# Kernel tuning notes

Hardware: AMD Instinct MI355X
Metric: run time of the kernel (lower is better)

Reference implementation:

```python
import jax, jax.numpy as jnp
import numpy as np

_THR = 0.008856  # OpenCV Lab threshold (6/29)^3


def _f_lab(t):
    # f(t) = t^(1/3) if t > thr else 7.787*t + 16/116 ; safe-where avoids nan/inf grads at 0
    safe = jnp.where(t > _THR, t, 1.0)
    return jnp.where(t > _THR, jnp.cbrt(safe), 7.787 * t + 16.0 / 116.0)


def _rgb_to_lab(img):
    """img: [B,3,H,W] in [0,1] -> OpenCV 8-bit-scaled Lab, divided by 255 (as in the torch code)."""
    img = jnp.clip(img, 0.0, 1.0)  # blur mixes channels so values can exceed 1; cv2 path saturates to 8-bit range
    r, g, b = img[:, 0], img[:, 1], img[:, 2]
    # linear RGB -> XYZ (OpenCV matrix), with white-point normalization of X and Z
    X = (0.412453 * r + 0.357580 * g + 0.180423 * b) / 0.950456
    Y = 0.212671 * r + 0.715160 * g + 0.072169 * b
    Z = (0.019334 * r + 0.119193 * g + 0.950227 * b) / 1.088754
    fX, fY, fZ = _f_lab(X), _f_lab(Y), _f_lab(Z)
    safeY = jnp.where(Y > _THR, Y, 1.0)
    L = jnp.where(Y > _THR, 116.0 * jnp.cbrt(safeY) - 16.0, 903.3 * Y)
    a = 500.0 * (fX - fY) + 128.0
    bb = 200.0 * (fY - fZ) + 128.0
    # OpenCV 8-bit scaling: L*255/100, a+128, b+128 ; torch code then divides by 255
    lab = jnp.stack([L * 255.0 / 100.0, a, bb], axis=1) / 255.0
    return lab


def _blur(img, weight):
    # F.conv2d with ones(3,3,5,5)/25, padding=2: each output channel is the SUM over input
    # channels of the 5x5 mean (full channel mixing, as in the torch module).
    return jax.lax.conv_general_dilated(
        img, weight, window_strides=(1, 1), padding=[(2, 2), (2, 2)],
        dimension_numbers=("NCHW", "OIHW", "NCHW"))


def setup_inputs() -> dict:
    key = jax.random.key(0)
    k1, k2 = jax.random.split(key)
    B, C, H, W = 32, 3, 512, 512
    img1 = jax.random.uniform(k1, (B, C, H, W), dtype=jnp.float32)
    img2 = jax.random.uniform(k2, (B, C, H, W), dtype=jnp.float32)
    kernel_size = 5
    weight = jnp.ones((3, 3, kernel_size, kernel_size), dtype=jnp.float32) / (kernel_size ** 2)
    return {"img1": img1, "img2": img2, "weight": weight}


def reference(img1, img2, weight):
    lab1 = _rgb_to_lab(_blur(img1, weight))
    lab2 = _rgb_to_lab(_blur(img2, weight))
    return jnp.mean((lab1 - lab2) ** 2)  # F.mse_loss, reduction='mean'
```

## Files before the change

### kernel.cpp

```cpp
#include <hip/hip_runtime.h>


constexpr int TILE  = 64;
constexpr int HALO  = 2;
constexpr int ROWS  = TILE + 2 * HALO;
constexpr int CPAD  = 72;
constexpr int NF4   = CPAD / 4;
constexpr int IMG_H = 512;
constexpr int IMG_W = 512;
constexpr int BATCH = 32;
constexpr float THR = 0.008856f;

__global__ __launch_bounds__(256, 8)
void lcol_mse_kernel(const float* __restrict__ img1,
                     const float* __restrict__ img2,
                     const float* __restrict__ weight,
                     float* __restrict__ out)
{
    __shared__ float cs[ROWS * CPAD];
    __shared__ float wpart[4];

    const int tid = threadIdx.x;
    const int bx0 = blockIdx.x * TILE;
    const int by0 = blockIdx.y * TILE;
    const int b   = blockIdx.z;
    const float wtap = weight[0];

    const size_t plane = (size_t)IMG_H * IMG_W;
    const float* bases[2] = { img1 + (size_t)b * 3 * plane,
                              img2 + (size_t)b * 3 * plane };

    const int x  = tid & 63;
    const int r0 = (tid >> 6) * 16;

    float L1[16];
    float acc = 0.f;

    for (int img = 0; img < 2; ++img) {
        const float* base = bases[img];

        for (int n = tid; n < ROWS * NF4; n += 256) {
            int row = n / NF4;
            int k   = n - row * NF4;
            int gy  = by0 + row - HALO;
            int gx  = bx0 + 4 * k - 4;
            float4 v = make_float4(0.f, 0.f, 0.f, 0.f);
            if ((unsigned)gy < (unsigned)IMG_H && (unsigned)gx < (unsigned)IMG_W) {
                const float* p = base + (size_t)gy * IMG_W + gx;
                float4 r  = *(const float4*)(p);
                float4 g  = *(const float4*)(p + plane);
                float4 bl = *(const float4*)(p + 2 * plane);
                v = make_float4(r.x + g.x + bl.x, r.y + g.y + bl.y,
                                r.z + g.z + bl.z, r.w + g.w + bl.w);
            }
            *(float4*)&cs[row * CPAD + 4 * k] = v;
        }
        __syncthreads();

        const float* colbase = &cs[x + 2];
        float h0 = colbase[(r0    ) * CPAD] + colbase[(r0    ) * CPAD + 1] + colbase[(r0    ) * CPAD + 2] + colbase[(r0    ) * CPAD + 3] + colbase[(r0    ) * CPAD + 4];
        float h1 = colbase[(r0 + 1) * CPAD] + colbase[(r0 + 1) * CPAD + 1] + colbase[(r0 + 1) * CPAD + 2] + colbase[(r0 + 1) * CPAD + 3] + colbase[(r0 + 1) * CPAD + 4];
        float h2 = colbase[(r0 + 2) * CPAD] + colbase[(r0 + 2) * CPAD + 1] + colbase[(r0 + 2) * CPAD + 2] + colbase[(r0 + 2) * CPAD + 3] + colbase[(r0 + 2) * CPAD + 4];
        float h3 = colbase[(r0 + 3) * CPAD] + colbase[(r0 + 3) * CPAD + 1] + colbase[(r0 + 3) * CPAD + 2] + colbase[(r0 + 3) * CPAD + 3] + colbase[(r0 + 3) * CPAD + 4];
        #pragma unroll
        for (int k = 0; k < 16; ++k) {
            const float* p = colbase + (r0 + 4 + k) * CPAD;
            float h4 = p[0] + p[1] + p[2] + p[3] + p[4];
            float v  = (h0 + h1 + h2 + h3 + h4) * wtap;
            v = fminf(fmaxf(v, 0.f), 1.f);
            float L = (v > THR) ? (116.f * cbrtf(v) - 16.f) : (903.3f * v);
            if (img == 0) L1[k] = L;
            else { float d = L1[k] - L; acc += d * d; }
            h0 = h1; h1 = h2; h2 = h3; h3 = h4;
        }
        __syncthreads();
    }

    #pragma unroll
    for (int off = 32; off; off >>= 1) acc += __shfl_down(acc, off);
    if ((tid & 63) == 0) wpart[tid >> 6] = acc;
    __syncthreads();
    if (tid == 0) {
        float s = wpart[0] + wpart[1] + wpart[2] + wpart[3];
        const float scale = (float)(1.0 / (10000.0 * (double)BATCH * 3.0 * IMG_H * IMG_W));
        atomicAdd(out, s * scale);
    }
}

extern "C" void kernel_launch(void* const* d_in, const int* in_sizes, int n_in,
                              void* d_out, int out_size, void* d_ws, size_t ws_size,
                              hipStream_t stream) {
    const float* img1   = (const float*)d_in[0];
    const float* img2   = (const float*)d_in[1];
    const float* weight = (const float*)d_in[2];
    float* out = (float*)d_out;

    hipMemsetAsync(out, 0, sizeof(float), stream);

    dim3 grid(IMG_W / TILE, IMG_H / TILE, BATCH);
    lcol_mse_kernel<<<grid, dim3(256), 0, stream>>>(img1, img2, weight, out);
}
```

Baseline: 235.0 us.

## Double-buffer LDS tiles and process two tiles per block with prefetch

Halves the grid so each block handles two tiles, which means four image-tile units per block. The shared-memory tile is double-buffered: global loads for the next unit are issued into registers before computing the current one, then written to the other buffer. This aims to hide global memory latency behind the cbrt/blur compute. In exchange it raises register pressure, lowers the occupancy target from 8 to 4 blocks per CU, and uses fewer blocks overall.

```diff
diff --git a/kernel.cpp b/kernel.cpp
--- a/kernel.cpp
+++ b/kernel.cpp
@@ -6,73 +6,122 @@
 constexpr int ROWS  = TILE + 2 * HALO;
 constexpr int CPAD  = 72;
 constexpr int NF4   = CPAD / 4;
+constexpr int NITER = ROWS * NF4;
 constexpr int IMG_H = 512;
 constexpr int IMG_W = 512;
 constexpr int BATCH = 32;
+constexpr int NBLOCKS = 1024;
 constexpr float THR = 0.008856f;
 
-__global__ __launch_bounds__(256, 8)
+__device__ __forceinline__ void issue_loads(const float* __restrict__ base,
+                                            int by0, int bx0, int tid,
+                                            float4 rv[5], float4 gv[5], float4 bv[5])
+{
+    const size_t plane = (size_t)IMG_H * IMG_W;
+    #pragma unroll
+    for (int k = 0; k < 5; ++k) {
+        int n    = tid + 256 * k;
+        int row  = n / NF4;
+        int col4 = (n - row * NF4) * 4;
+        int gy   = by0 + row - HALO;
+        int gx   = bx0 + col4 - 4;
+        float4 z = make_float4(0.f, 0.f, 0.f, 0.f);
+        rv[k] = z; gv[k] = z; bv[k] = z;
+        if (n < NITER && (unsigned)gy < (unsigned)IMG_H && (unsigned)gx < (unsigned)IMG_W) {
+            const float* p = base + (size_t)gy * IMG_W + gx;
+            rv[k] = *(const float4*)(p);
+            gv[k] = *(const float4*)(p + plane);
+            bv[k] = *(const float4*)(p + 2 * plane);
+        }
+    }
+}
+
+__device__ __forceinline__ void write_stage(float* __restrict__ buf, int tid,
+                                            const float4 rv[5], const float4 gv[5],
+                                            const float4 bv[5])
+{
+    #pragma unroll
+    for (int k = 0; k < 5; ++k) {
+        int n = tid + 256 * k;
+        if (n < NITER) {
+            int row  = n / NF4;
+            int col4 = (n - row * NF4) * 4;
+            float4 v;
+            v.x = rv[k].x + gv[k].x + bv[k].x;
+            v.y = rv[k].y + gv[k].y + bv[k].y;
+            v.z = rv[k].z + gv[k].z + bv[k].z;
+            v.w = rv[k].w + gv[k].w + bv[k].w;
+            *(float4*)&buf[row * CPAD + col4] = v;
+        }
+    }
+}
+
+__device__ __forceinline__ void compute_unit(const float* __restrict__ buf,
+                                             int x, int r0, float wtap, bool first,
+                                             float L1[16], float& acc)
+{
+    const float* colbase = buf + x + 2;
+    float h0 = colbase[(r0    ) * CPAD] + colbase[(r0    ) * CPAD + 1] + colbase[(r0    ) * CPAD + 2] + colbase[(r0    ) * CPAD + 3] + colbase[(r0    ) * CPAD + 4];
+    float h1 = colbase[(r0 + 1) * CPAD] + colbase[(r0 + 1) * CPAD + 1] + colbase[(r0 + 1) * CPAD + 2] + colbase[(r0 + 1) * CPAD + 3] + colbase[(r0 + 1) * CPAD + 4];
+    float h2 = colbase[(r0 + 2) * CPAD] + colbase[(r0 + 2) * CPAD + 1] + colbase[(r0 + 2) * CPAD + 2] + colbase[(r0 + 2) * CPAD + 3] + colbase[(r0 + 2) * CPAD + 4];
+    float h3 = colbase[(r0 + 3) * CPAD] + colbase[(r0 + 3) * CPAD + 1] + colbase[(r0 + 3) * CPAD + 2] + colbase[(r0 + 3) * CPAD + 3] + colbase[(r0 + 3) * CPAD + 4];
+    #pragma unroll
+    for (int k = 0; k < 16; ++k) {
+        const float* p = colbase + (r0 + 4 + k) * CPAD;
+        float h4 = p[0] + p[1] + p[2] + p[3] + p[4];
+        float v  = (h0 + h1 + h2 + h3 + h4) * wtap;
+        v = fminf(fmaxf(v, 0.f), 1.f);
+        float L = (v > THR) ? (116.f * cbrtf(v) - 16.f) : (903.3f * v);
+        if (first) L1[k] = L;
+        else { float d = L1[k] - L; acc += d * d; }
+        h0 = h1; h1 = h2; h2 = h3; h3 = h4;
+    }
+}
+
+__global__ __launch_bounds__(256, 4)
 void lcol_mse_kernel(const float* __restrict__ img1,
                      const float* __restrict__ img2,
                      const float* __restrict__ weight,
                      float* __restrict__ out)
 {
-    __shared__ float cs[ROWS * CPAD];
+    __shared__ float cs[2][ROWS * CPAD];
     __shared__ float wpart[4];
 
     const int tid = threadIdx.x;
-    const int bx0 = blockIdx.x * TILE;
-    const int by0 = blockIdx.y * TILE;
-    const int b   = blockIdx.z;
+    const int x   = tid & 63;
+    const int r0  = (tid >> 6) * 16;
     const float wtap = weight[0];
+    const size_t plane = (size_t)IMG_H * IMG_W;
 
-    const size_t plane = (size_t)IMG_H * IMG_W;
-    const float* bases[2] = { img1 + (size_t)b * 3 * plane,
-                              img2 + (size_t)b * 3 * plane };
-
-    const int x  = tid & 63;
-    const int r0 = (tid >> 6) * 16;
+    int by0s[2], bx0s[2];
+    const float* bases[4];
+    #pragma unroll
+    for (int t = 0; t < 2; ++t) {
+        int tile = (int)blockIdx.x + t * NBLOCKS;
+        int b    = tile >> 6;
+        int rem  = tile & 63;
+        by0s[t]  = (rem >> 3) * TILE;
+        bx0s[t]  = (rem & 7) * TILE;
+        bases[2 * t]     = img1 + (size_t)b * 3 * plane;
+        bases[2 * t + 1] = img2 + (size_t)b * 3 * plane;
+    }
 
     float L1[16];
     float acc = 0.f;
+    float4 rv[5], gv[5], bv[5];
 
-    for (int img = 0; img < 2; ++img) {
-        const float* base = bases[img];
+    issue_loads(bases[0], by0s[0], bx0s[0], tid, rv, gv, bv);
+    write_stage(cs[0], tid, rv, gv, bv);
+    __syncthreads();
 
-        for (int n = tid; n < ROWS * NF4; n += 256) {
-            int row = n / NF4;
-            int k   = n - row * NF4;
-            int gy  = by0 + row - HALO;
-            int gx  = bx0 + 4 * k - 4;
-            float4 v = make_float4(0.f, 0.f, 0.f, 0.f);
-            if ((unsigned)gy < (unsigned)IMG_H && (unsigned)gx < (unsigned)IMG_W) {
-                const float* p = base + (size_t)gy * IMG_W + gx;
-                float4 r  = *(const float4*)(p);
-                float4 g  = *(const float4*)(p + plane);
-                float4 bl = *(const float4*)(p + 2 * plane);
-                v = make_float4(r.x + g.x + bl.x, r.y + g.y + bl.y,
-                                r.z + g.z + bl.z, r.w + g.w + bl.w);
-            }
-            *(float4*)&cs[row * CPAD + 4 * k] = v;
-        }
-        __syncthreads();
-
-        const float* colbase = &cs[x + 2];
-        float h0 = colbase[(r0    ) * CPAD] + colbase[(r0    ) * CPAD + 1] + colbase[(r0    ) * CPAD + 2] + colbase[(r0    ) * CPAD + 3] + colbase[(r0    ) * CPAD + 4];
-        float h1 = colbase[(r0 + 1) * CPAD] + colbase[(r0 + 1) * CPAD + 1] + colbase[(r0 + 1) * CPAD + 2] + colbase[(r0 + 1) * CPAD + 3] + colbase[(r0 + 1) * CPAD + 4];
-        float h2 = colbase[(r0 + 2) * CPAD] + colbase[(r0 + 2) * CPAD + 1] + colbase[(r0 + 2) * CPAD + 2] + colbase[(r0 + 2) * CPAD + 3] + colbase[(r0 + 2) * CPAD + 4];
-        float h3 = colbase[(r0 + 3) * CPAD] + colbase[(r0 + 3) * CPAD + 1] + colbase[(r0 + 3) * CPAD + 2] + colbase[(r0 + 3) * CPAD + 3] + colbase[(r0 + 3) * CPAD + 4];
-        #pragma unroll
-        for (int k = 0; k < 16; ++k) {
-            const float* p = colbase + (r0 + 4 + k) * CPAD;
-            float h4 = p[0] + p[1] + p[2] + p[3] + p[4];
-            float v  = (h0 + h1 + h2 + h3 + h4) * wtap;
-            v = fminf(fmaxf(v, 0.f), 1.f);
-            float L = (v > THR) ? (116.f * cbrtf(v) - 16.f) : (903.3f * v);
-            if (img == 0) L1[k] = L;
-            else { float d = L1[k] - L; acc += d * d; }
-            h0 = h1; h1 = h2; h2 = h3; h3 = h4;
-        }
+    #pragma unroll
+    for (int u = 0; u < 4; ++u) {
+        if (u < 3)
+            issue_loads(bases[u + 1], by0s[(u + 1) >> 1], bx0s[(u + 1) >> 1],
+                        tid, rv, gv, bv);
+        compute_unit(cs[u & 1], x, r0, wtap, (u & 1) == 0, L1, acc);
+        if (u < 3)
+            write_stage(cs[(u + 1) & 1], tid, rv, gv, bv);
         __syncthreads();
     }
 
@@ -97,6 +146,5 @@
 
     hipMemsetAsync(out, 0, sizeof(float), stream);
 
-    dim3 grid(IMG_W / TILE, IMG_H / TILE, BATCH);
-    lcol_mse_kernel<<<grid, dim3(256), 0, stream>>>(img1, img2, weight, out);
+    lcol_mse_kernel<<<dim3(NBLOCKS), dim3(256), 0, stream>>>(img1, img2, weight, out);
 }
```

Measured after the change: 228.5 us. 2.8% less time.
